# Optimization experiments

Hardware: AMD Instinct MI355X
Metric: run time of the kernel (lower is better)

## Reference

```python
import jax, jax.numpy as jnp
import numpy as np

B, T, NF, D = 512, 24, 81, 64
NH, HD = 4, 16
EPS = 1e-5


def _ln(x, g, b):
    m = x.mean(-1, keepdims=True)
    v = ((x - m) ** 2).mean(-1, keepdims=True)
    return (x - m) * jax.lax.rsqrt(v + EPS) * g + b


def _glu(h, w1, b1, w2, b2):
    return jax.nn.sigmoid(h @ w1 + b1) * (h @ w2 + b2)


def setup_inputs() -> dict:
    key = jax.random.key(0)
    ki = iter(jax.random.split(key, 64))

    def w(*shape):
        return jax.random.normal(next(ki), shape, jnp.float32) * 0.05

    FD = NF * D
    inp = {
        "x": jax.random.normal(next(ki), (B, T, NF), jnp.float32),
        # 81 per-feature GRNs, stacked along axis 0 (feature axis)
        "f_w1": w(NF, D), "f_b1": w(NF, D),
        "f_w2": w(NF, D, D), "f_b2": w(NF, D),
        "f_g1w": w(NF, D, D), "f_g1b": w(NF, D),
        "f_g2w": w(NF, D, D), "f_g2b": w(NF, D),
        "f_skw": w(NF, D), "f_skb": w(NF, D),
        "f_lng": jnp.ones((NF, D), jnp.float32), "f_lnb": jnp.zeros((NF, D), jnp.float32),
        # weight GRN: 5184 -> 64 -> 81
        "w_w1": w(FD, D), "w_b1": w(D),
        "w_w2": w(D, NF), "w_b2": w(NF),
        "w_g1w": w(NF, NF), "w_g1b": w(NF),
        "w_g2w": w(NF, NF), "w_g2b": w(NF),
        "w_skw": w(FD, NF), "w_skb": w(NF),
        "w_lng": jnp.ones((NF,), jnp.float32), "w_lnb": jnp.zeros((NF,), jnp.float32),
        # LSTM (torch layout: [4H, in], gate order i,f,g,o)
        "lstm_wih": w(4 * D, D), "lstm_whh": w(4 * D, D),
        "lstm_bih": w(4 * D), "lstm_bhh": w(4 * D),
        # post-lstm GLU + LN
        "pl_g1w": w(D, D), "pl_g1b": w(D), "pl_g2w": w(D, D), "pl_g2b": w(D),
        "pl_lng": jnp.ones((D,), jnp.float32), "pl_lnb": jnp.zeros((D,), jnp.float32),
        # MHA (in-proj packed q,k,v; weights stored [in, out])
        "attn_in_w": w(D, 3 * D), "attn_in_b": w(3 * D),
        "attn_out_w": w(D, D), "attn_out_b": w(D),
        # post-attn GLU + LN
        "pa_g1w": w(D, D), "pa_g1b": w(D), "pa_g2w": w(D, D), "pa_g2b": w(D),
        "pa_lng": jnp.ones((D,), jnp.float32), "pa_lnb": jnp.zeros((D,), jnp.float32),
        # feed-forward GRN (skip = identity since d_in == d_out)
        "ff_w1": w(D, 2 * D), "ff_b1": w(2 * D),
        "ff_w2": w(2 * D, D), "ff_b2": w(D),
        "ff_g1w": w(D, D), "ff_g1b": w(D), "ff_g2w": w(D, D), "ff_g2b": w(D),
        "ff_lng": jnp.ones((D,), jnp.float32), "ff_lnb": jnp.zeros((D,), jnp.float32),
        # output head
        "fc1_w": w(D, D), "fc1_b": w(D),
        "fc2_w": w(D, 6), "fc2_b": w(6),
    }
    return inp


def _forward(x, f_w1, f_b1, f_w2, f_b2, f_g1w, f_g1b, f_g2w, f_g2b, f_skw, f_skb,
             f_lng, f_lnb,
             w_w1, w_b1, w_w2, w_b2, w_g1w, w_g1b, w_g2w, w_g2b, w_skw, w_skb,
             w_lng, w_lnb,
             lstm_wih, lstm_whh, lstm_bih, lstm_bhh,
             pl_g1w, pl_g1b, pl_g2w, pl_g2b, pl_lng, pl_lnb,
             attn_in_w, attn_in_b, attn_out_w, attn_out_b,
             pa_g1w, pa_g1b, pa_g2w, pa_g2b, pa_lng, pa_lnb,
             ff_w1, ff_b1, ff_w2, ff_b2, ff_g1w, ff_g1b, ff_g2w, ff_g2b,
             ff_lng, ff_lnb,
             fc1_w, fc1_b, fc2_w, fc2_b):
    Bv, Tv = x.shape[0], x.shape[1]
    # --- VSN: 81 per-feature GRNs, vectorized over the feature axis ---
    h = jax.nn.elu(x[..., None] * f_w1 + f_b1)                    # [B,T,F,D]
    h = jnp.einsum('btfi,fio->btfo', h, f_w2) + f_b2
    h = jax.nn.sigmoid(jnp.einsum('btfi,fio->btfo', h, f_g1w) + f_g1b) \
        * (jnp.einsum('btfi,fio->btfo', h, f_g2w) + f_g2b)
    res = x[..., None] * f_skw + f_skb                            # skip: Linear(1,D)
    stacked = _ln(h + res, f_lng, f_lnb)                          # [B,T,F,D]
    flat = stacked.reshape(Bv, Tv, NF * D)
    # weight GRN -> softmax over features
    wh = jax.nn.elu(flat @ w_w1 + w_b1)
    wh = wh @ w_w2 + w_b2
    wh = _glu(wh, w_g1w, w_g1b, w_g2w, w_g2b)
    wnorm = _ln(wh + flat @ w_skw + w_skb, w_lng, w_lnb)
    weights = jax.nn.softmax(wnorm, axis=-1)                      # [B,T,F]
    selected = jnp.einsum('btfd,btf->btd', stacked, weights)      # [B,T,D]

    # --- LSTM encoder (single layer) ---
    def step(carry, xt):
        hp, cp = carry
        gates = xt @ lstm_wih.T + hp @ lstm_whh.T + lstm_bih + lstm_bhh
        i, f, g, o = jnp.split(gates, 4, axis=-1)
        c = jax.nn.sigmoid(f) * cp + jax.nn.sigmoid(i) * jnp.tanh(g)
        hn = jax.nn.sigmoid(o) * jnp.tanh(c)
        return (hn, c), hn

    h0 = jnp.zeros((Bv, D), x.dtype)
    _, hs = jax.lax.scan(step, (h0, h0), selected.transpose(1, 0, 2))
    lstm_out = hs.transpose(1, 0, 2)                              # [B,T,D]

    temporal = _ln(_glu(lstm_out, pl_g1w, pl_g1b, pl_g2w, pl_g2b) + selected,
                   pl_lng, pl_lnb)

    # --- Multi-head self-attention ---
    qkv = temporal @ attn_in_w + attn_in_b                        # [B,T,3D]
    q, k, v = jnp.split(qkv, 3, axis=-1)

    def heads(t):
        return t.reshape(Bv, Tv, NH, HD).transpose(0, 2, 1, 3)

    q, k, v = heads(q), heads(k), heads(v)
    scores = jnp.einsum('bhqd,bhkd->bhqk', q, k) / jnp.sqrt(jnp.float32(HD))
    a = jax.nn.softmax(scores, axis=-1)
    ao = jnp.einsum('bhqk,bhkd->bhqd', a, v).transpose(0, 2, 1, 3).reshape(Bv, Tv, D)
    attn_out = ao @ attn_out_w + attn_out_b

    enriched = _ln(_glu(attn_out, pa_g1w, pa_g1b, pa_g2w, pa_g2b) + temporal,
                   pa_lng, pa_lnb)

    # --- FF GRN (identity skip) ---
    fh = jax.nn.elu(enriched @ ff_w1 + ff_b1)
    fh = fh @ ff_w2 + ff_b2
    fh = _glu(fh, ff_g1w, ff_g1b, ff_g2w, ff_g2b)
    out = _ln(fh + enriched, ff_lng, ff_lnb)

    pooled = out.mean(axis=1)                                     # [B,D]
    return jax.nn.relu(pooled @ fc1_w + fc1_b) @ fc2_w + fc2_b    # [B,6]


def reference(x, f_w1, f_b1, f_w2, f_b2, f_g1w, f_g1b, f_g2w, f_g2b, f_skw, f_skb,
              f_lng, f_lnb,
              w_w1, w_b1, w_w2, w_b2, w_g1w, w_g1b, w_g2w, w_g2b, w_skw, w_skb,
              w_lng, w_lnb,
              lstm_wih, lstm_whh, lstm_bih, lstm_bhh,
              pl_g1w, pl_g1b, pl_g2w, pl_g2b, pl_lng, pl_lnb,
              attn_in_w, attn_in_b, attn_out_w, attn_out_b,
              pa_g1w, pa_g1b, pa_g2w, pa_g2b, pa_lng, pa_lnb,
              ff_w1, ff_b1, ff_w2, ff_b2, ff_g1w, ff_g1b, ff_g2w, ff_g2b,
              ff_lng, ff_lnb,
              fc1_w, fc1_b, fc2_w, fc2_b):
    return _forward(x, f_w1, f_b1, f_w2, f_b2, f_g1w, f_g1b, f_g2w, f_g2b, f_skw,
                    f_skb, f_lng, f_lnb, w_w1, w_b1, w_w2, w_b2, w_g1w, w_g1b,
                    w_g2w, w_g2b, w_skw, w_skb, w_lng, w_lnb, lstm_wih, lstm_whh,
                    lstm_bih, lstm_bhh, pl_g1w, pl_g1b, pl_g2w, pl_g2b, pl_lng,
                    pl_lnb, attn_in_w, attn_in_b, attn_out_w, attn_out_b, pa_g1w,
                    pa_g1b, pa_g2w, pa_g2b, pa_lng, pa_lnb, ff_w1, ff_b1, ff_w2,
                    ff_b2, ff_g1w, ff_g1b, ff_g2w, ff_g2b, ff_lng, ff_lnb, fc1_w,
                    fc1_b, fc2_w, fc2_b)
```

## Files before the change

kernel.cpp:

```cpp
#include <hip/hip_runtime.h>
#include <hip/hip_bf16.h>
#include <math.h>

constexpr int BB   = 512;
constexpr int TSEQ = 24;
constexpr int NF   = 81;
constexpr int DD   = 64;
constexpr int MTOT = BB * TSEQ;
constexpr int FDIM = NF * DD;
constexpr int KS   = 6;
constexpr int KSL  = 864;
constexpr int NW   = 160;
constexpr int NT   = 6;
constexpr float LN_EPS = 1e-5f;

typedef __attribute__((ext_vector_type(8))) short short8v;
typedef __attribute__((ext_vector_type(4))) float f32x4;

static __device__ __forceinline__ float sigmoidf_(float x) {
    return __builtin_amdgcn_rcpf(1.f + __expf(-x));
}
static __device__ __forceinline__ float eluf_(float x) {
    return x > 0.f ? x : (__expf(x) - 1.f);
}
// ... 403 lines not shown
            for (int rg = 0; rg < 4; ++rg)
                acc[rg][cf] = __builtin_amdgcn_mfma_f32_16x16x32_bf16(af[rg], bf, acc[rg][cf], 0, 0, 0);
        }
    }
    #pragma unroll
    for (int rg = 0; rg < 4; ++rg)
        #pragma unroll
        for (int cf = 0; cf < 4; ++cf)
            #pragma unroll
            for (int j = 0; j < 4; ++j) {
                int r = rg*16 + lg*4 + j, c = w*64 + cf*16 + lr;
                xW[(size_t)(m0 + r) * 256 + c] = acc[rg][cf][j] + vbs[c];
            }
}

__global__ void lstm_prep_kernel(
    const float* __restrict__ whh, float* __restrict__ whhT)
{
    int id = blockIdx.x * 256 + threadIdx.x;
    if (id < 16384) {
        int i = id >> 8, j = id & 255;
        whhT[id] = whh[j*64 + i];
    }
}

__global__ __launch_bounds__(256) void lstm_kernel(
    const float* __restrict__ xW, const float* __restrict__ whhT,
    float* __restrict__ out)
{
    __shared__ float sh[64];
    __shared__ float sg[256];
    const int t = threadIdx.x;
    const int b = blockIdx.x;

    float wreg[64];
    #pragma unroll
    for (int i = 0; i < 64; ++i) wreg[i] = whhT[i*256 + t];

    if (t < 64) sh[t] = 0.f;
    float c_reg = 0.f;

    float xnext = xW[((size_t)b * TSEQ + 0) * 256 + t];
    __syncthreads();

    for (int tt = 0; tt < TSEQ; ++tt) {
        float acc = xnext;
        if (tt + 1 < TSEQ)
            xnext = xW[((size_t)b * TSEQ + tt + 1) * 256 + t];
        #pragma unroll
        for (int i = 0; i < 64; ++i) acc += sh[i] * wreg[i];
        sg[t] = acc;
        __syncthreads();
        if (t < 64) {
            float gi = sg[t], gf = sg[64 + t], gg = sg[128 + t], go = sg[192 + t];
            c_reg = sigmoidf_(gf) * c_reg + sigmoidf_(gi) * ftanh_(gg);
            float hn = sigmoidf_(go) * ftanh_(c_reg);
            sh[t] = hn;
            out[((size_t)b * TSEQ + tt) * 64 + t] = hn;
        }
        __syncthreads();
    }
}

__global__ __launch_bounds__(256) void fused_pl_qkv_kernel(
    const float* __restrict__ in, const float* __restrict__ res,
    const float* __restrict__ g1w, const float* __restrict__ g1b,
    const float* __restrict__ g2w, const float* __restrict__ g2b,
    const float* __restrict__ lng, const float* __restrict__ lnb,
    const float* __restrict__ wqkv, const float* __restrict__ bqkv,
    float* __restrict__ outf, float* __restrict__ qkv)
{
    const int m0 = blockIdx.x * 32;
    const int t = threadIdx.x;
    const int w = t >> 6, l = t & 63, lr = l & 15, lg = l >> 4;
    __shared__ __align__(16) unsigned short hA[32 * 72];
    __shared__ __align__(16) unsigned char U[27648];
    unsigned short* Wt0 = (unsigned short*)U;
    unsigned short* Wt1 = (unsigned short*)(U + 9216);
    float* yA = (float*)U;
    unsigned short* Wq = (unsigned short*)U;
    __shared__ float vg1b[64], vg2b[64], vlng[64], vlnb[64], vbq[192];

    if (t < 64) { vg1b[t] = g1b[t]; vg2b[t] = g2b[t]; vlng[t] = lng[t]; vlnb[t] = lnb[t]; }
    if (t < 192) vbq[t] = bqkv[t];
    #pragma unroll
    for (int p = 0; p < 8; ++p) {
        int e = t + 256 * p; int r = e >> 6, d = e & 63;
        hA[r*72 + d] = f2bf(in[(size_t)(m0 + r) * 64 + d]);
    }
    #pragma unroll
    for (int p = 0; p < 16; ++p) {
        int e = t + 256 * p; int k = e >> 6, c = e & 63;
        Wt0[c*72 + k] = f2bf(g1w[k*64 + c]);
        Wt1[c*72 + k] = f2bf(g2w[k*64 + c]);
    }
    __syncthreads();

    f32x4 aA[2], aB[2];
    #pragma unroll
    for (int rg = 0; rg < 2; ++rg) { aA[rg] = (f32x4){0.f,0.f,0.f,0.f}; aB[rg] = (f32x4){0.f,0.f,0.f,0.f}; }
    #pragma unroll
    for (int ks = 0; ks < 2; ++ks) {
        short8v b0f = *(const short8v*)&Wt0[(w*16 + lr)*72 + ks*32 + lg*8];
        short8v b1f = *(const short8v*)&Wt1[(w*16 + lr)*72 + ks*32 + lg*8];
        #pragma unroll
        for (int rg = 0; rg < 2; ++rg) {
            short8v af = *(const short8v*)&hA[(rg*16 + lr)*72 + ks*32 + lg*8];
            aA[rg] = __builtin_amdgcn_mfma_f32_16x16x32_bf16(af, b0f, aA[rg], 0, 0, 0);
            aB[rg] = __builtin_amdgcn_mfma_f32_16x16x32_bf16(af, b1f, aB[rg], 0, 0, 0);
        }
    }
    float yv[2][4];
    #pragma unroll
    for (int rg = 0; rg < 2; ++rg)
        #pragma unroll
        for (int j = 0; j < 4; ++j) {
            int r = rg*16 + lg*4 + j, c = w*16 + lr;
            float sg = sigmoidf_(aA[rg][j] + vg1b[c]);
            yv[rg][j] = sg * (aB[rg][j] + vg2b[c]) + res[(size_t)(m0 + r) * 64 + c];
        }
    __syncthreads();

    #pragma unroll
    for (int rg = 0; rg < 2; ++rg)
        #pragma unroll
        for (int j = 0; j < 4; ++j) {
            int r = rg*16 + lg*4 + j, c = w*16 + lr;
            yA[r*68 + c] = yv[rg][j];
        }
    __syncthreads();

    const int tr = t >> 4, tc = t & 15;
    #pragma unroll
    for (int a = 0; a < 2; ++a) {
        const int r = tr + 16*a;
        float4 v4 = *(const float4*)&yA[r*68 + tc*4];
        float part = v4.x + v4.y + v4.z + v4.w;
        #pragma unroll
        for (int off = 1; off < 16; off <<= 1) part += __shfl_xor(part, off);
        const float mean = part * (1.f / 64.f);
        float d0 = v4.x - mean, d1 = v4.y - mean, d2 = v4.z - mean, d3 = v4.w - mean;
        float vp = d0*d0 + d1*d1 + d2*d2 + d3*d3;
        #pragma unroll
        for (int off = 1; off < 16; off <<= 1) vp += __shfl_xor(vp, off);
        const float inv = rsqrtf(vp * (1.f / 64.f) + LN_EPS);
        const int c0 = tc * 4;
        float4 ov;
        ov.x = d0 * inv * vlng[c0+0] + vlnb[c0+0];
        ov.y = d1 * inv * vlng[c0+1] + vlnb[c0+1];
        ov.z = d2 * inv * vlng[c0+2] + vlnb[c0+2];
        ov.w = d3 * inv * vlng[c0+3] + vlnb[c0+3];
        *(float4*)&outf[(size_t)(m0 + r) * 64 + c0] = ov;
        ushort4 ob;
        ob.x = f2bf(ov.x); ob.y = f2bf(ov.y); ob.z = f2bf(ov.z); ob.w = f2bf(ov.w);
        *(ushort4*)&hA[r*72 + c0] = ob;
    }
    __syncthreads();

    #pragma unroll
    for (int p = 0; p < 48; ++p) {
        int e = t + 256 * p; int c = e >> 6, k = e & 63;
        Wq[c*72 + k] = f2bf(wqkv[(size_t)k * 192 + c]);
    }
    __syncthreads();

    f32x4 acc[2][3];
    #pragma unroll
    for (int rg = 0; rg < 2; ++rg)
        #pragma unroll
        for (int cf = 0; cf < 3; ++cf) acc[rg][cf] = (f32x4){0.f,0.f,0.f,0.f};
    #pragma unroll
    for (int ks = 0; ks < 2; ++ks) {
        short8v af[2];
        #pragma unroll
        for (int rg = 0; rg < 2; ++rg)
            af[rg] = *(const short8v*)&hA[(rg*16 + lr)*72 + ks*32 + lg*8];
        #pragma unroll
        for (int cf = 0; cf < 3; ++cf) {
            short8v bf = *(const short8v*)&Wq[(w*48 + cf*16 + lr)*72 + ks*32 + lg*8];
            #pragma unroll
            for (int rg = 0; rg < 2; ++rg)
                acc[rg][cf] = __builtin_amdgcn_mfma_f32_16x16x32_bf16(af[rg], bf, acc[rg][cf], 0, 0, 0);
        }
    }
    #pragma unroll
    for (int rg = 0; rg < 2; ++rg)
        #pragma unroll
        for (int cf = 0; cf < 3; ++cf)
            #pragma unroll
            for (int j = 0; j < 4; ++j) {
                int r = rg*16 + lg*4 + j, c = w*48 + cf*16 + lr;
                qkv[(size_t)(m0 + r) * 192 + c] = acc[rg][cf][j] + vbq[c];
            }
}

__global__ __launch_bounds__(256) void attn_kernel(
    const float* __restrict__ qkv, __hip_bfloat16* __restrict__ ao)
{
    const int b = blockIdx.x;
    const int h = threadIdx.x >> 6, l = threadIdx.x & 63;
    __shared__ float sq[4][24][16], sk[4][24][16], sv[4][24][16], sp[4][24][24];
    #pragma unroll
    for (int p = 0; p < 6; ++p) {
        int e = l + 64 * p; int ti = e >> 4, d = e & 15;
        size_t base = ((size_t)(b * TSEQ + ti)) * 192 + h * 16 + d;
        sq[h][ti][d] = qkv[base];
        sk[h][ti][d] = qkv[base + 64];
        sv[h][ti][d] = qkv[base + 128];
    }
    __syncthreads();
    #pragma unroll
    for (int p = 0; p < 9; ++p) {
        int e = l + 64 * p; int i = e / 24, j = e - i * 24;
        float s = 0.f;
        #pragma unroll
        for (int d = 0; d < 16; ++d) s += sq[h][i][d] * sk[h][j][d];
        sp[h][i][j] = s * 0.25f;
    }
    __syncthreads();
    if (l < 24) {
        float mx = -1e30f;
        for (int j = 0; j < 24; ++j) mx = fmaxf(mx, sp[h][l][j]);
        float s = 0.f;
        for (int j = 0; j < 24; ++j) { float e = __expf(sp[h][l][j] - mx); sp[h][l][j] = e; s += e; }
        float inv = __builtin_amdgcn_rcpf(s);
        for (int j = 0; j < 24; ++j) sp[h][l][j] *= inv;
    }
    __syncthreads();
    #pragma unroll
    for (int p = 0; p < 6; ++p) {
        int e = l + 64 * p; int ti = e >> 4, d = e & 15;
        float s = 0.f;
        #pragma unroll
        for (int j = 0; j < 24; ++j) s += sp[h][ti][j] * sv[h][j][d];
        ao[((size_t)(b * TSEQ + ti)) * 64 + h * 16 + d] = __float2bfloat16(s);
    }
}

__global__ __launch_bounds__(256) void fused_paff_kernel(
    const __hip_bfloat16* __restrict__ ao, const float* __restrict__ res_t,
    const float* __restrict__ wout, const float* __restrict__ bout,
    const float* __restrict__ pg1w, const float* __restrict__ pg1b,
    const float* __restrict__ pg2w, const float* __restrict__ pg2b,
    const float* __restrict__ plng, const float* __restrict__ plnb,
    const float* __restrict__ fw1, const float* __restrict__ fb1,
    const float* __restrict__ fw2, const float* __restrict__ fb2,
    const float* __restrict__ fg1w, const float* __restrict__ fg1b,
    const float* __restrict__ fg2w, const float* __restrict__ fg2b,
    const float* __restrict__ flng, const float* __restrict__ flnb,
    float* __restrict__ escratch, float* __restrict__ outln)
{
    const int m0 = blockIdx.x * 32;
    const int t = threadIdx.x;
    const int w = t >> 6, l = t & 63, lr = l & 15, lg = l >> 4;
    __shared__ __align__(16) unsigned short hA[32 * 72];
    __shared__ __align__(16) unsigned short hB[32 * 136];
    __shared__ __align__(16) unsigned char U1[18432];
    __shared__ __align__(16) unsigned char U2[17408];
    unsigned short* Wt0 = (unsigned short*)U1;
    unsigned short* Wt1 = (unsigned short*)(U1 + 9216);
    unsigned short* W1t = (unsigned short*)U1;
    unsigned short* W2t = (unsigned short*)U2;
    float* yA = (float*)U2;
    __shared__ float vob[64], vp1b[64], vp2b[64], vplg[64], vplb[64];
    __shared__ float vf1b[128], vf2b[64], vfg1b[64], vfg2b[64], vflg[64], vflb[64];

    if (t < 64) {
        vob[t] = bout[t]; vp1b[t] = pg1b[t]; vp2b[t] = pg2b[t];
        vplg[t] = plng[t]; vplb[t] = plnb[t];
        vf2b[t] = fb2[t]; vfg1b[t] = fg1b[t]; vfg2b[t] = fg2b[t];
        vflg[t] = flng[t]; vflb[t] = flnb[t];
    }
    if (t < 128) vf1b[t] = fb1[t];
    #pragma unroll
    for (int p = 0; p < 8; ++p) {
        int e = t + 256 * p; int r = e >> 6, d = e & 63;
        hA[r*72 + d] = *(const unsigned short*)&ao[(size_t)(m0 + r) * 64 + d];
    }
    #pragma unroll
    for (int p = 0; p < 16; ++p) {
        int e = t + 256 * p; int k = e >> 6, c = e & 63;
        Wt0[c*72 + k] = f2bf(wout[k*64 + c]);
    }
    __syncthreads();

    f32x4 acc1[2];
    #pragma unroll
    for (int rg = 0; rg < 2; ++rg) acc1[rg] = (f32x4){0.f,0.f,0.f,0.f};
    #pragma unroll
    for (int ks = 0; ks < 2; ++ks) {
        short8v bf = *(const short8v*)&Wt0[(w*16 + lr)*72 + ks*32 + lg*8];
        #pragma unroll
        for (int rg = 0; rg < 2; ++rg) {
            short8v af = *(const short8v*)&hA[(rg*16 + lr)*72 + ks*32 + lg*8];
            acc1[rg] = __builtin_amdgcn_mfma_f32_16x16x32_bf16(af, bf, acc1[rg], 0, 0, 0);
        }
    }
    #pragma unroll
    for (int p = 0; p < 16; ++p) {
        int e = t + 256 * p; int k = e >> 6, c = e & 63;
        Wt1[c*72 + k] = f2bf(pg1w[k*64 + c]);
    }
    __syncthreads();

    #pragma unroll
    for (int rg = 0; rg < 2; ++rg)
        #pragma unroll
        for (int j = 0; j < 4; ++j) {
            int r = rg*16 + lg*4 + j, c = w*16 + lr;
            hA[r*72 + c] = f2bf(acc1[rg][j] + vob[c]);
        }
    #pragma unroll
    for (int p = 0; p < 16; ++p) {
        int e = t + 256 * p; int k = e >> 6, c = e & 63;
        Wt0[c*72 + k] = f2bf(pg2w[k*64 + c]);
    }
    __syncthreads();

    f32x4 aA[2], aB[2];
    #pragma unroll
    for (int rg = 0; rg < 2; ++rg) { aA[rg] = (f32x4){0.f,0.f,0.f,0.f}; aB[rg] = (f32x4){0.f,0.f,0.f,0.f}; }
    #pragma unroll
    for (int ks = 0; ks < 2; ++ks) {
        short8v b1f = *(const short8v*)&Wt1[(w*16 + lr)*72 + ks*32 + lg*8];
        short8v b2f = *(const short8v*)&Wt0[(w*16 + lr)*72 + ks*32 + lg*8];
        #pragma unroll
        for (int rg = 0; rg < 2; ++rg) {
            short8v af = *(const short8v*)&hA[(rg*16 + lr)*72 + ks*32 + lg*8];
            aA[rg] = __builtin_amdgcn_mfma_f32_16x16x32_bf16(af, b1f, aA[rg], 0, 0, 0);
            aB[rg] = __builtin_amdgcn_mfma_f32_16x16x32_bf16(af, b2f, aB[rg], 0, 0, 0);
        }
    }
    float yv[2][4];
    #pragma unroll
    for (int rg = 0; rg < 2; ++rg)
        #pragma unroll
        for (int j = 0; j < 4; ++j) {
            int r = rg*16 + lg*4 + j, c = w*16 + lr;
            float sg = sigmoidf_(aA[rg][j] + vp1b[c]);
            yv[rg][j] = sg * (aB[rg][j] + vp2b[c]) + res_t[(size_t)(m0 + r) * 64 + c];
        }
    __syncthreads();

    #pragma unroll
    for (int rg = 0; rg < 2; ++rg)
        #pragma unroll
        for (int j = 0; j < 4; ++j) {
            int r = rg*16 + lg*4 + j, c = w*16 + lr;
            yA[r*68 + c] = yv[rg][j];
        }
    __syncthreads();

    const int tr = t >> 4, tc = t & 15;
    #pragma unroll
    for (int a = 0; a < 2; ++a) {
        const int r = tr + 16*a;
        float4 v4 = *(const float4*)&yA[r*68 + tc*4];
        float part = v4.x + v4.y + v4.z + v4.w;
        #pragma unroll
        for (int off = 1; off < 16; off <<= 1) part += __shfl_xor(part, off);
        const float mean = part * (1.f / 64.f);
        float d0 = v4.x - mean, d1 = v4.y - mean, d2 = v4.z - mean, d3 = v4.w - mean;
        float vp = d0*d0 + d1*d1 + d2*d2 + d3*d3;
        #pragma unroll
        for (int off = 1; off < 16; off <<= 1) vp += __shfl_xor(vp, off);
        const float inv = rsqrtf(vp * (1.f / 64.f) + LN_EPS);
        const int c0 = tc * 4;
        float4 ov;
        ov.x = d0 * inv * vplg[c0+0] + vplb[c0+0];
        ov.y = d1 * inv * vplg[c0+1] + vplb[c0+1];
        ov.z = d2 * inv * vplg[c0+2] + vplb[c0+2];
        ov.w = d3 * inv * vplg[c0+3] + vplb[c0+3];
        *(float4*)&escratch[(size_t)(m0 + r) * 64 + c0] = ov;
        ushort4 ob;
        ob.x = f2bf(ov.x); ob.y = f2bf(ov.y); ob.z = f2bf(ov.z); ob.w = f2bf(ov.w);
        *(ushort4*)&hA[r*72 + c0] = ob;
    }
    __syncthreads();

    #pragma unroll
    for (int p = 0; p < 32; ++p) {
        int e = t + 256 * p; int k = e >> 7, c = e & 127;
        W1t[c*72 + k] = f2bf(fw1[(size_t)k * 128 + c]);
    }
    __syncthreads();

    f32x4 accf[2][2];
    #pragma unroll
// ... 65 lines not shown
    for (int ks = 0; ks < 2; ++ks) {
        short8v b1f = *(const short8v*)&Wt0[(w*16 + lr)*72 + ks*32 + lg*8];
        short8v b2f = *(const short8v*)&Wt1[(w*16 + lr)*72 + ks*32 + lg*8];
        #pragma unroll
        for (int rg = 0; rg < 2; ++rg) {
            short8v af = *(const short8v*)&hA[(rg*16 + lr)*72 + ks*32 + lg*8];
            aA[rg] = __builtin_amdgcn_mfma_f32_16x16x32_bf16(af, b1f, aA[rg], 0, 0, 0);
            aB[rg] = __builtin_amdgcn_mfma_f32_16x16x32_bf16(af, b2f, aB[rg], 0, 0, 0);
        }
    }
    #pragma unroll
    for (int rg = 0; rg < 2; ++rg)
        #pragma unroll
        for (int j = 0; j < 4; ++j) {
            int r = rg*16 + lg*4 + j, c = w*16 + lr;
            float sg = sigmoidf_(aA[rg][j] + vfg1b[c]);
            yv[rg][j] = sg * (aB[rg][j] + vfg2b[c]) + escratch[(size_t)(m0 + r) * 64 + c];
        }
    __syncthreads();

    #pragma unroll
    for (int rg = 0; rg < 2; ++rg)
        #pragma unroll
        for (int j = 0; j < 4; ++j) {
            int r = rg*16 + lg*4 + j, c = w*16 + lr;
            yA[r*68 + c] = yv[rg][j];
        }
    __syncthreads();

    #pragma unroll
    for (int a = 0; a < 2; ++a) {
        const int r = tr + 16*a;
// ... 1 lines not shown
        float part = v4.x + v4.y + v4.z + v4.w;
        #pragma unroll
        for (int off = 1; off < 16; off <<= 1) part += __shfl_xor(part, off);
        const float mean = part * (1.f / 64.f);
        float d0 = v4.x - mean, d1 = v4.y - mean, d2 = v4.z - mean, d3 = v4.w - mean;
        float vp = d0*d0 + d1*d1 + d2*d2 + d3*d3;
        #pragma unroll
        for (int off = 1; off < 16; off <<= 1) vp += __shfl_xor(vp, off);
        const float inv = rsqrtf(vp * (1.f / 64.f) + LN_EPS);
        const int c0 = tc * 4;
        float4 ov;
        ov.x = d0 * inv * vflg[c0+0] + vflb[c0+0];
        ov.y = d1 * inv * vflg[c0+1] + vflb[c0+1];
        ov.z = d2 * inv * vflg[c0+2] + vflb[c0+2];
        ov.w = d3 * inv * vflg[c0+3] + vflb[c0+3];
        *(float4*)&outln[(size_t)(m0 + r) * 64 + c0] = ov;
    }
}

__global__ __launch_bounds__(64) void head_kernel(
    const float* __restrict__ outln,
    const float* __restrict__ fc1_w, const float* __restrict__ fc1_b,
    const float* __restrict__ fc2_w, const float* __restrict__ fc2_b,
    float* __restrict__ out)
{
    const int b = blockIdx.x, l = threadIdx.x;
    __shared__ float sp[64];
    float s = 0.f;
    #pragma unroll
    for (int tt = 0; tt < TSEQ; ++tt) s += outln[((size_t)(b * TSEQ + tt)) * 64 + l];
    sp[l] = s * (1.f / 24.f);
    __syncthreads();
    float a = fc1_b[l];
    for (int k = 0; k < 64; ++k) a += sp[k] * fc1_w[k*64 + l];
    float f1 = fmaxf(a, 0.f);
    #pragma unroll
    for (int j = 0; j < 6; ++j) {
        float p = f1 * fc2_w[l*6 + j];
        #pragma unroll
        for (int off = 32; off; off >>= 1) p += __shfl_xor(p, off);
        if (l == 0) out[b*6 + j] = p + fc2_b[j];
    }
}

extern "C" void kernel_launch(void* const* d_in, const int* in_sizes, int n_in,
                              void* d_out, int out_size, void* d_ws, size_t ws_size,
                              hipStream_t stream)
{
    const float* x        = (const float*)d_in[0];
    const float* f_w1     = (const float*)d_in[1];
    const float* f_b1     = (const float*)d_in[2];
    const float* f_w2     = (const float*)d_in[3];
    const float* f_b2     = (const float*)d_in[4];
    const float* f_g1w    = (const float*)d_in[5];
    const float* f_g1b    = (const float*)d_in[6];
    const float* f_g2w    = (const float*)d_in[7];
// ... 41 lines not shown
    const float* ff_g1w   = (const float*)d_in[49];
    const float* ff_g1b   = (const float*)d_in[50];
    const float* ff_g2w   = (const float*)d_in[51];
    const float* ff_g2b   = (const float*)d_in[52];
    const float* ff_lng   = (const float*)d_in[53];
    const float* ff_lnb   = (const float*)d_in[54];
    const float* fc1_w    = (const float*)d_in[55];
    const float* fc1_b    = (const float*)d_in[56];
    const float* fc2_w    = (const float*)d_in[57];
    const float* fc2_b    = (const float*)d_in[58];

    float* ws = (float*)d_ws;

    size_t o = 0;
    const size_t o_S0   = o; o += (size_t)MTOT * 256;
    const size_t o_A    = o; o += (size_t)MTOT * 64;
    const size_t o_Bf   = o; o += (size_t)MTOT * 64;
    const size_t o_Cf   = o; o += (size_t)MTOT * 64;
    const size_t o_Df   = o; o += (size_t)MTOT * 64;
    const size_t o_F    = o; o += (size_t)MTOT * 128;
    const size_t o_whhT = o; o += 16384;
    const size_t unionP2 = o;

    const size_t o_ab = o_F;

    const size_t persist = (size_t)MTOT * 177;
    int mc = 0;
    {
        const int cands[4] = {12288, 6144, 3072, 1536};
        for (int ci = 0; ci < 4; ++ci) {
            const size_t c = (size_t)cands[ci];
            size_t overlay = c * FDIM / 2 + (size_t)KS * c * NW + c * 81
                           + (size_t)NW * FDIM / 2;
            size_t A = overlay > unionP2 ? overlay : unionP2;
            if ((A + persist) * sizeof(float) <= ws_size) { mc = cands[ci]; break; }
        }
        if (mc == 0) return;
    }
    const size_t ovl_partial = (size_t)mc * FDIM / 2;
// ... 13 lines not shown

    for (int mb = 0; mb < MTOT; mb += mc) {
        __hip_bfloat16* chunk = (__hip_bfloat16*)ws;
        vsn_kernel<<<dim3((mc / 64) / NT, NF), blk, 0, stream>>>(
            ws + o_xt + mb, f_w1, f_b1, f_w2, f_b2, f_g1w, f_g1b,
            f_g2w, f_g2b, f_skw, f_skb, f_lng, f_lnb, chunk);
        wgemm_kernel<<<dim3(mc / 32, KS), dim3(64), 0, stream>>>(
            chunk, (const unsigned short*)(ws + ovl_wcat), ws + ovl_partial, mc);
        wtail_kernel<<<dim3(mc / 16), blk, 0, stream>>>(
            ws + ovl_partial, chunk, w_b1, w_skb, w_w2, w_b2, w_g1w, w_g1b,
            w_g2w, w_g2b, w_lng, w_lnb,
            ws + o_sel + (size_t)mb * 64,
            (__hip_bfloat16*)(ws + o_selb) + (size_t)mb * 64, mc);
    }

    lstm_prep_kernel<<<dim3(64), blk, 0, stream>>>(lstm_whh, ws + o_whhT);
    xw_kernel<<<dim3(MTOT / 64), blk, 0, stream>>>(
        (const __hip_bfloat16*)(ws + o_selb), lstm_wih, lstm_bih, lstm_bhh, ws + o_S0);
    lstm_kernel<<<dim3(BB), blk, 0, stream>>>(ws + o_S0, ws + o_whhT, ws + o_A);
    fused_pl_qkv_kernel<<<dim3(MTOT / 32), blk, 0, stream>>>(
        ws + o_A, ws + o_sel, pl_g1w, pl_g1b, pl_g2w, pl_g2b, pl_lng, pl_lnb,
        attn_in_w, attn_in_b, ws + o_Df, ws + o_S0);
    attn_kernel<<<dim3(BB), blk, 0, stream>>>(
        ws + o_S0, (__hip_bfloat16*)(ws + o_ab));
    fused_paff_kernel<<<dim3(MTOT / 32), blk, 0, stream>>>(
        (const __hip_bfloat16*)(ws + o_ab), ws + o_Df,
        attn_out_w, attn_out_b, pa_g1w, pa_g1b, pa_g2w, pa_g2b, pa_lng, pa_lnb,
        ff_w1, ff_b1, ff_w2, ff_b2, ff_g1w, ff_g1b, ff_g2w, ff_g2b,
        ff_lng, ff_lnb, ws + o_Bf, ws + o_Cf);
    head_kernel<<<dim3(BB), dim3(64), 0, stream>>>(
        ws + o_Cf, fc1_w, fc1_b, fc2_w, fc2_b, (float*)d_out);
}
```

Before: 355.6 us.

## Fuse LSTM, post-LSTM GLU, attention, feed-forward and head into one per-batch kernel

Replaces five kernels (LSTM, post-LSTM GLU+QKV, attention, post-attention/FF GRN, head) with one kernel that runs one block per batch element and keeps every intermediate in shared memory. The hidden state goes straight into a bf16 tile padded to 32 rows, and residuals stay in LDS, so the global round trips and launches between stages disappear. It also drops the separate W_hh transpose kernel by loading W_hh rows directly into registers. In exchange only 512 blocks do the dense GEMM stages (previously 384 blocks of 32 rows each), and the larger LDS footprint plus 64 weight registers per thread may reduce occupancy. Every block also reconverts all the weight matrices.

```diff
diff --git a/kernel.cpp b/kernel.cpp
--- a/kernel.cpp
+++ b/kernel.cpp
@@ -441,39 +441,76 @@
             }
 }
 
-__global__ void lstm_prep_kernel(
-    const float* __restrict__ whh, float* __restrict__ whhT)
-{
-    int id = blockIdx.x * 256 + threadIdx.x;
-    if (id < 16384) {
-        int i = id >> 8, j = id & 255;
-        whhT[id] = whh[j*64 + i];
-    }
-}
-
-__global__ __launch_bounds__(256) void lstm_kernel(
-    const float* __restrict__ xW, const float* __restrict__ whhT,
+__global__ __launch_bounds__(256) void batch_kernel(
+    const float* __restrict__ xW, const float* __restrict__ whh,
+    const float* __restrict__ sel,
+    const float* __restrict__ pg1w, const float* __restrict__ pg1b,
+    const float* __restrict__ pg2w, const float* __restrict__ pg2b,
+    const float* __restrict__ plng, const float* __restrict__ plnb,
+    const float* __restrict__ wqkv, const float* __restrict__ bqkv,
+    const float* __restrict__ wout, const float* __restrict__ bout,
+    const float* __restrict__ ag1w, const float* __restrict__ ag1b,
+    const float* __restrict__ ag2w, const float* __restrict__ ag2b,
+    const float* __restrict__ alng, const float* __restrict__ alnb,
+    const float* __restrict__ fw1, const float* __restrict__ fb1,
+    const float* __restrict__ fw2, const float* __restrict__ fb2,
+    const float* __restrict__ fg1w, const float* __restrict__ fg1b,
+    const float* __restrict__ fg2w, const float* __restrict__ fg2b,
+    const float* __restrict__ flng, const float* __restrict__ flnb,
+    const float* __restrict__ fc1_w, const float* __restrict__ fc1_b,
+    const float* __restrict__ fc2_w, const float* __restrict__ fc2_b,
     float* __restrict__ out)
 {
-    __shared__ float sh[64];
-    __shared__ float sg[256];
-    const int t = threadIdx.x;
-    const int b = blockIdx.x;
+    const int b  = blockIdx.x;
+    const int m0 = b * TSEQ;
+    const int t  = threadIdx.x;
+    const int w  = t >> 6, l = t & 63, lr = l & 15, lg = l >> 4;
+    const int tr = t >> 4, tc = t & 15;
+
+    __shared__ float tmp[32 * 68];
+    __shared__ float enr[32 * 68];
+    __shared__ __align__(16) unsigned short hA[32 * 72];
+    __shared__ __align__(16) unsigned short hB[32 * 136];
+    __shared__ __align__(16) unsigned char U[35840];
+    __shared__ float sh[64], sg[256];
+    __shared__ float vpg1b[64], vpg2b[64], vplg[64], vplb[64], vbq[192];
+    __shared__ float vob[64], vag1b[64], vag2b[64], valg[64], valb[64];
+    __shared__ float vf1b[128], vf2b[64], vfg1b[64], vfg2b[64], vflg[64], vflb[64];
+
+    unsigned short* Wt0 = (unsigned short*)U;
+    unsigned short* Wt1 = (unsigned short*)(U + 9216);
+    float*          yA  = (float*)(U + 18432);
+    unsigned short* Wq  = (unsigned short*)U;
+    float* sq = (float*)U;
+    float* sk = (float*)(U + 6144);
+    float* sv = (float*)(U + 12288);
+    float* sp = (float*)(U + 18432);
+    unsigned short* W1t = (unsigned short*)U;
+    unsigned short* W2t = (unsigned short*)(U + 18432);
+
+    if (t < 64) {
+        vpg1b[t] = pg1b[t]; vpg2b[t] = pg2b[t]; vplg[t] = plng[t]; vplb[t] = plnb[t];
+        vob[t] = bout[t]; vag1b[t] = ag1b[t]; vag2b[t] = ag2b[t];
+        valg[t] = alng[t]; valb[t] = alnb[t];
+        vf2b[t] = fb2[t]; vfg1b[t] = fg1b[t]; vfg2b[t] = fg2b[t];
+        vflg[t] = flng[t]; vflb[t] = flnb[t];
+    }
+    if (t < 192) vbq[t] = bqkv[t];
+    if (t < 128) vf1b[t] = fb1[t];
+    for (int e = t; e < 8 * 72; e += 256) hA[24*72 + e] = 0;
 
     float wreg[64];
     #pragma unroll
-    for (int i = 0; i < 64; ++i) wreg[i] = whhT[i*256 + t];
-
+    for (int i = 0; i < 64; ++i) wreg[i] = whh[t*64 + i];
     if (t < 64) sh[t] = 0.f;
     float c_reg = 0.f;
-
-    float xnext = xW[((size_t)b * TSEQ + 0) * 256 + t];
+    float xnext = xW[(size_t)m0 * 256 + t];
     __syncthreads();
 
     for (int tt = 0; tt < TSEQ; ++tt) {
         float acc = xnext;
         if (tt + 1 < TSEQ)
-            xnext = xW[((size_t)b * TSEQ + tt + 1) * 256 + t];
+            xnext = xW[(size_t)(m0 + tt + 1) * 256 + t];
         #pragma unroll
         for (int i = 0; i < 64; ++i) acc += sh[i] * wreg[i];
         sg[t] = acc;
@@ -483,43 +520,16 @@
             c_reg = sigmoidf_(gf) * c_reg + sigmoidf_(gi) * ftanh_(gg);
             float hn = sigmoidf_(go) * ftanh_(c_reg);
             sh[t] = hn;
-            out[((size_t)b * TSEQ + tt) * 64 + t] = hn;
+            hA[tt*72 + t] = f2bf(hn);
         }
         __syncthreads();
     }
-}
-
-__global__ __launch_bounds__(256) void fused_pl_qkv_kernel(
-    const float* __restrict__ in, const float* __restrict__ res,
-    const float* __restrict__ g1w, const float* __restrict__ g1b,
-    const float* __restrict__ g2w, const float* __restrict__ g2b,
-    const float* __restrict__ lng, const float* __restrict__ lnb,
-    const float* __restrict__ wqkv, const float* __restrict__ bqkv,
-    float* __restrict__ outf, float* __restrict__ qkv)
-{
-    const int m0 = blockIdx.x * 32;
-    const int t = threadIdx.x;
-    const int w = t >> 6, l = t & 63, lr = l & 15, lg = l >> 4;
-    __shared__ __align__(16) unsigned short hA[32 * 72];
-    __shared__ __align__(16) unsigned char U[27648];
-    unsigned short* Wt0 = (unsigned short*)U;
-    unsigned short* Wt1 = (unsigned short*)(U + 9216);
-    float* yA = (float*)U;
-    unsigned short* Wq = (unsigned short*)U;
-    __shared__ float vg1b[64], vg2b[64], vlng[64], vlnb[64], vbq[192];
-
-    if (t < 64) { vg1b[t] = g1b[t]; vg2b[t] = g2b[t]; vlng[t] = lng[t]; vlnb[t] = lnb[t]; }
-    if (t < 192) vbq[t] = bqkv[t];
-    #pragma unroll
-    for (int p = 0; p < 8; ++p) {
-        int e = t + 256 * p; int r = e >> 6, d = e & 63;
-        hA[r*72 + d] = f2bf(in[(size_t)(m0 + r) * 64 + d]);
-    }
+
     #pragma unroll
     for (int p = 0; p < 16; ++p) {
         int e = t + 256 * p; int k = e >> 6, c = e & 63;
-        Wt0[c*72 + k] = f2bf(g1w[k*64 + c]);
-        Wt1[c*72 + k] = f2bf(g2w[k*64 + c]);
+        Wt0[c*72 + k] = f2bf(pg1w[k*64 + c]);
+        Wt1[c*72 + k] = f2bf(pg2w[k*64 + c]);
     }
     __syncthreads();
 
@@ -543,8 +553,9 @@
         #pragma unroll
         for (int j = 0; j < 4; ++j) {
             int r = rg*16 + lg*4 + j, c = w*16 + lr;
-            float sg = sigmoidf_(aA[rg][j] + vg1b[c]);
-            yv[rg][j] = sg * (aB[rg][j] + vg2b[c]) + res[(size_t)(m0 + r) * 64 + c];
+            size_t rrow = (size_t)(m0 + r); if (rrow >= MTOT) rrow = MTOT - 1;
+            float sgv = sigmoidf_(aA[rg][j] + vpg1b[c]);
+            yv[rg][j] = sgv * (aB[rg][j] + vpg2b[c]) + sel[rrow * 64 + c];
         }
     __syncthreads();
 
@@ -557,228 +568,6 @@
         }
     __syncthreads();
 
-    const int tr = t >> 4, tc = t & 15;
-    #pragma unroll
-    for (int a = 0; a < 2; ++a) {
-        const int r = tr + 16*a;
-        float4 v4 = *(const float4*)&yA[r*68 + tc*4];
-        float part = v4.x + v4.y + v4.z + v4.w;
-        #pragma unroll
-        for (int off = 1; off < 16; off <<= 1) part += __shfl_xor(part, off);
-        const float mean = part * (1.f / 64.f);
-        float d0 = v4.x - mean, d1 = v4.y - mean, d2 = v4.z - mean, d3 = v4.w - mean;
-        float vp = d0*d0 + d1*d1 + d2*d2 + d3*d3;
-        #pragma unroll
-        for (int off = 1; off < 16; off <<= 1) vp += __shfl_xor(vp, off);
-        const float inv = rsqrtf(vp * (1.f / 64.f) + LN_EPS);
-        const int c0 = tc * 4;
-        float4 ov;
-        ov.x = d0 * inv * vlng[c0+0] + vlnb[c0+0];
-        ov.y = d1 * inv * vlng[c0+1] + vlnb[c0+1];
-        ov.z = d2 * inv * vlng[c0+2] + vlnb[c0+2];
-        ov.w = d3 * inv * vlng[c0+3] + vlnb[c0+3];
-        *(float4*)&outf[(size_t)(m0 + r) * 64 + c0] = ov;
-        ushort4 ob;
-        ob.x = f2bf(ov.x); ob.y = f2bf(ov.y); ob.z = f2bf(ov.z); ob.w = f2bf(ov.w);
-        *(ushort4*)&hA[r*72 + c0] = ob;
-    }
-    __syncthreads();
-
-    #pragma unroll
-    for (int p = 0; p < 48; ++p) {
-        int e = t + 256 * p; int c = e >> 6, k = e & 63;
-        Wq[c*72 + k] = f2bf(wqkv[(size_t)k * 192 + c]);
-    }
-    __syncthreads();
-
-    f32x4 acc[2][3];
-    #pragma unroll
-    for (int rg = 0; rg < 2; ++rg)
-        #pragma unroll
-        for (int cf = 0; cf < 3; ++cf) acc[rg][cf] = (f32x4){0.f,0.f,0.f,0.f};
-    #pragma unroll
-    for (int ks = 0; ks < 2; ++ks) {
-        short8v af[2];
-        #pragma unroll
-        for (int rg = 0; rg < 2; ++rg)
-            af[rg] = *(const short8v*)&hA[(rg*16 + lr)*72 + ks*32 + lg*8];
-        #pragma unroll
-        for (int cf = 0; cf < 3; ++cf) {
-            short8v bf = *(const short8v*)&Wq[(w*48 + cf*16 + lr)*72 + ks*32 + lg*8];
-            #pragma unroll
-            for (int rg = 0; rg < 2; ++rg)
-                acc[rg][cf] = __builtin_amdgcn_mfma_f32_16x16x32_bf16(af[rg], bf, acc[rg][cf], 0, 0, 0);
-        }
-    }
-    #pragma unroll
-    for (int rg = 0; rg < 2; ++rg)
-        #pragma unroll
-        for (int cf = 0; cf < 3; ++cf)
-            #pragma unroll
-            for (int j = 0; j < 4; ++j) {
-                int r = rg*16 + lg*4 + j, c = w*48 + cf*16 + lr;
-                qkv[(size_t)(m0 + r) * 192 + c] = acc[rg][cf][j] + vbq[c];
-            }
-}
-
-__global__ __launch_bounds__(256) void attn_kernel(
-    const float* __restrict__ qkv, __hip_bfloat16* __restrict__ ao)
-{
-    const int b = blockIdx.x;
-    const int h = threadIdx.x >> 6, l = threadIdx.x & 63;
-    __shared__ float sq[4][24][16], sk[4][24][16], sv[4][24][16], sp[4][24][24];
-    #pragma unroll
-    for (int p = 0; p < 6; ++p) {
-        int e = l + 64 * p; int ti = e >> 4, d = e & 15;
-        size_t base = ((size_t)(b * TSEQ + ti)) * 192 + h * 16 + d;
-        sq[h][ti][d] = qkv[base];
-        sk[h][ti][d] = qkv[base + 64];
-        sv[h][ti][d] = qkv[base + 128];
-    }
-    __syncthreads();
-    #pragma unroll
-    for (int p = 0; p < 9; ++p) {
-        int e = l + 64 * p; int i = e / 24, j = e - i * 24;
-        float s = 0.f;
-        #pragma unroll
-        for (int d = 0; d < 16; ++d) s += sq[h][i][d] * sk[h][j][d];
-        sp[h][i][j] = s * 0.25f;
-    }
-    __syncthreads();
-    if (l < 24) {
-        float mx = -1e30f;
-        for (int j = 0; j < 24; ++j) mx = fmaxf(mx, sp[h][l][j]);
-        float s = 0.f;
-        for (int j = 0; j < 24; ++j) { float e = __expf(sp[h][l][j] - mx); sp[h][l][j] = e; s += e; }
-        float inv = __builtin_amdgcn_rcpf(s);
-        for (int j = 0; j < 24; ++j) sp[h][l][j] *= inv;
-    }
-    __syncthreads();
-    #pragma unroll
-    for (int p = 0; p < 6; ++p) {
-        int e = l + 64 * p; int ti = e >> 4, d = e & 15;
-        float s = 0.f;
-        #pragma unroll
-        for (int j = 0; j < 24; ++j) s += sp[h][ti][j] * sv[h][j][d];
-        ao[((size_t)(b * TSEQ + ti)) * 64 + h * 16 + d] = __float2bfloat16(s);
-    }
-}
-
-__global__ __launch_bounds__(256) void fused_paff_kernel(
-    const __hip_bfloat16* __restrict__ ao, const float* __restrict__ res_t,
-    const float* __restrict__ wout, const float* __restrict__ bout,
-    const float* __restrict__ pg1w, const float* __restrict__ pg1b,
-    const float* __restrict__ pg2w, const float* __restrict__ pg2b,
-    const float* __restrict__ plng, const float* __restrict__ plnb,
-    const float* __restrict__ fw1, const float* __restrict__ fb1,
-    const float* __restrict__ fw2, const float* __restrict__ fb2,
-    const float* __restrict__ fg1w, const float* __restrict__ fg1b,
-    const float* __restrict__ fg2w, const float* __restrict__ fg2b,
-    const float* __restrict__ flng, const float* __restrict__ flnb,
-    float* __restrict__ escratch, float* __restrict__ outln)
-{
-    const int m0 = blockIdx.x * 32;
-    const int t = threadIdx.x;
-    const int w = t >> 6, l = t & 63, lr = l & 15, lg = l >> 4;
-    __shared__ __align__(16) unsigned short hA[32 * 72];
-    __shared__ __align__(16) unsigned short hB[32 * 136];
-    __shared__ __align__(16) unsigned char U1[18432];
-    __shared__ __align__(16) unsigned char U2[17408];
-    unsigned short* Wt0 = (unsigned short*)U1;
-    unsigned short* Wt1 = (unsigned short*)(U1 + 9216);
-    unsigned short* W1t = (unsigned short*)U1;
-    unsigned short* W2t = (unsigned short*)U2;
-    float* yA = (float*)U2;
-    __shared__ float vob[64], vp1b[64], vp2b[64], vplg[64], vplb[64];
-    __shared__ float vf1b[128], vf2b[64], vfg1b[64], vfg2b[64], vflg[64], vflb[64];
-
-    if (t < 64) {
-        vob[t] = bout[t]; vp1b[t] = pg1b[t]; vp2b[t] = pg2b[t];
-        vplg[t] = plng[t]; vplb[t] = plnb[t];
-        vf2b[t] = fb2[t]; vfg1b[t] = fg1b[t]; vfg2b[t] = fg2b[t];
-        vflg[t] = flng[t]; vflb[t] = flnb[t];
-    }
-    if (t < 128) vf1b[t] = fb1[t];
-    #pragma unroll
-    for (int p = 0; p < 8; ++p) {
-        int e = t + 256 * p; int r = e >> 6, d = e & 63;
-        hA[r*72 + d] = *(const unsigned short*)&ao[(size_t)(m0 + r) * 64 + d];
-    }
-    #pragma unroll
-    for (int p = 0; p < 16; ++p) {
-        int e = t + 256 * p; int k = e >> 6, c = e & 63;
-        Wt0[c*72 + k] = f2bf(wout[k*64 + c]);
-    }
-    __syncthreads();
-
-    f32x4 acc1[2];
-    #pragma unroll
-    for (int rg = 0; rg < 2; ++rg) acc1[rg] = (f32x4){0.f,0.f,0.f,0.f};
-    #pragma unroll
-    for (int ks = 0; ks < 2; ++ks) {
-        short8v bf = *(const short8v*)&Wt0[(w*16 + lr)*72 + ks*32 + lg*8];
-        #pragma unroll
-        for (int rg = 0; rg < 2; ++rg) {
-            short8v af = *(const short8v*)&hA[(rg*16 + lr)*72 + ks*32 + lg*8];
-            acc1[rg] = __builtin_amdgcn_mfma_f32_16x16x32_bf16(af, bf, acc1[rg], 0, 0, 0);
-        }
-    }
-    #pragma unroll
-    for (int p = 0; p < 16; ++p) {
-        int e = t + 256 * p; int k = e >> 6, c = e & 63;
-        Wt1[c*72 + k] = f2bf(pg1w[k*64 + c]);
-    }
-    __syncthreads();
-
-    #pragma unroll
-    for (int rg = 0; rg < 2; ++rg)
-        #pragma unroll
-        for (int j = 0; j < 4; ++j) {
-            int r = rg*16 + lg*4 + j, c = w*16 + lr;
-            hA[r*72 + c] = f2bf(acc1[rg][j] + vob[c]);
-        }
-    #pragma unroll
-    for (int p = 0; p < 16; ++p) {
-        int e = t + 256 * p; int k = e >> 6, c = e & 63;
-        Wt0[c*72 + k] = f2bf(pg2w[k*64 + c]);
-    }
-    __syncthreads();
-
-    f32x4 aA[2], aB[2];
-    #pragma unroll
-    for (int rg = 0; rg < 2; ++rg) { aA[rg] = (f32x4){0.f,0.f,0.f,0.f}; aB[rg] = (f32x4){0.f,0.f,0.f,0.f}; }
-    #pragma unroll
-    for (int ks = 0; ks < 2; ++ks) {
-        short8v b1f = *(const short8v*)&Wt1[(w*16 + lr)*72 + ks*32 + lg*8];
-        short8v b2f = *(const short8v*)&Wt0[(w*16 + lr)*72 + ks*32 + lg*8];
-        #pragma unroll
-        for (int rg = 0; rg < 2; ++rg) {
-            short8v af = *(const short8v*)&hA[(rg*16 + lr)*72 + ks*32 + lg*8];
-            aA[rg] = __builtin_amdgcn_mfma_f32_16x16x32_bf16(af, b1f, aA[rg], 0, 0, 0);
-            aB[rg] = __builtin_amdgcn_mfma_f32_16x16x32_bf16(af, b2f, aB[rg], 0, 0, 0);
-        }
-    }
-    float yv[2][4];
-    #pragma unroll
-    for (int rg = 0; rg < 2; ++rg)
-        #pragma unroll
-        for (int j = 0; j < 4; ++j) {
-            int r = rg*16 + lg*4 + j, c = w*16 + lr;
-            float sg = sigmoidf_(aA[rg][j] + vp1b[c]);
-            yv[rg][j] = sg * (aB[rg][j] + vp2b[c]) + res_t[(size_t)(m0 + r) * 64 + c];
-        }
-    __syncthreads();
-
-    #pragma unroll
-    for (int rg = 0; rg < 2; ++rg)
-        #pragma unroll
-        for (int j = 0; j < 4; ++j) {
-            int r = rg*16 + lg*4 + j, c = w*16 + lr;
-            yA[r*68 + c] = yv[rg][j];
-        }
-    __syncthreads();
-
-    const int tr = t >> 4, tc = t & 15;
     #pragma unroll
     for (int a = 0; a < 2; ++a) {
         const int r = tr + 16*a;
@@ -798,7 +587,177 @@
         ov.y = d1 * inv * vplg[c0+1] + vplb[c0+1];
         ov.z = d2 * inv * vplg[c0+2] + vplb[c0+2];
         ov.w = d3 * inv * vplg[c0+3] + vplb[c0+3];
-        *(float4*)&escratch[(size_t)(m0 + r) * 64 + c0] = ov;
+        *(float4*)&tmp[r*68 + c0] = ov;
+        ushort4 ob;
+        ob.x = f2bf(ov.x); ob.y = f2bf(ov.y); ob.z = f2bf(ov.z); ob.w = f2bf(ov.w);
+        *(ushort4*)&hA[r*72 + c0] = ob;
+    }
+    __syncthreads();
+
+    #pragma unroll
+    for (int p = 0; p < 48; ++p) {
+        int e = t + 256 * p; int c = e >> 6, k = e & 63;
+        Wq[c*72 + k] = f2bf(wqkv[(size_t)k * 192 + c]);
+    }
+    __syncthreads();
+
+    f32x4 accq[2][3];
+    #pragma unroll
+    for (int rg = 0; rg < 2; ++rg)
+        #pragma unroll
+        for (int cf = 0; cf < 3; ++cf) accq[rg][cf] = (f32x4){0.f,0.f,0.f,0.f};
+    #pragma unroll
+    for (int ks = 0; ks < 2; ++ks) {
+        short8v af[2];
+        #pragma unroll
+        for (int rg = 0; rg < 2; ++rg)
+            af[rg] = *(const short8v*)&hA[(rg*16 + lr)*72 + ks*32 + lg*8];
+        #pragma unroll
+        for (int cf = 0; cf < 3; ++cf) {
+            short8v bf = *(const short8v*)&Wq[(w*48 + cf*16 + lr)*72 + ks*32 + lg*8];
+            #pragma unroll
+            for (int rg = 0; rg < 2; ++rg)
+                accq[rg][cf] = __builtin_amdgcn_mfma_f32_16x16x32_bf16(af[rg], bf, accq[rg][cf], 0, 0, 0);
+        }
+    }
+    __syncthreads();
+
+    #pragma unroll
+    for (int rg = 0; rg < 2; ++rg)
+        #pragma unroll
+        for (int cf = 0; cf < 3; ++cf)
+            #pragma unroll
+            for (int j = 0; j < 4; ++j) {
+                int r = rg*16 + lg*4 + j, c = w*48 + cf*16 + lr;
+                if (r < TSEQ) {
+                    float val = accq[rg][cf][j] + vbq[c];
+                    int seg = c >> 6, hh = (c & 63) >> 4, dd = c & 15;
+                    float* dst = (seg == 0) ? sq : (seg == 1 ? sk : sv);
+                    dst[(hh*24 + r)*16 + dd] = val;
+                }
+            }
+    __syncthreads();
+
+    #pragma unroll
+    for (int p = 0; p < 9; ++p) {
+        int e = l + 64 * p; int i = e / 24, j2 = e - i * 24;
+        float s = 0.f;
+        #pragma unroll
+        for (int d = 0; d < 16; ++d) s += sq[(w*24 + i)*16 + d] * sk[(w*24 + j2)*16 + d];
+        sp[(w*24 + i)*24 + j2] = s * 0.25f;
+    }
+    __syncthreads();
+    if (l < 24) {
+        float mx = -1e30f;
+        for (int j = 0; j < 24; ++j) mx = fmaxf(mx, sp[(w*24 + l)*24 + j]);
+        float s = 0.f;
+        for (int j = 0; j < 24; ++j) { float e = __expf(sp[(w*24 + l)*24 + j] - mx); sp[(w*24 + l)*24 + j] = e; s += e; }
+        float inv = __builtin_amdgcn_rcpf(s);
+        for (int j = 0; j < 24; ++j) sp[(w*24 + l)*24 + j] *= inv;
+    }
+    __syncthreads();
+    #pragma unroll
+    for (int p = 0; p < 6; ++p) {
+        int e = l + 64 * p; int ti = e >> 4, d = e & 15;
+        float s = 0.f;
+        #pragma unroll
+        for (int j = 0; j < 24; ++j) s += sp[(w*24 + ti)*24 + j] * sv[(w*24 + j)*16 + d];
+        hA[ti*72 + w*16 + d] = f2bf(s);
+    }
+    __syncthreads();
+
+    #pragma unroll
+    for (int p = 0; p < 16; ++p) {
+        int e = t + 256 * p; int k = e >> 6, c = e & 63;
+        Wt0[c*72 + k] = f2bf(wout[k*64 + c]);
+    }
+    __syncthreads();
+
+    f32x4 acc1[2];
+    #pragma unroll
+    for (int rg = 0; rg < 2; ++rg) acc1[rg] = (f32x4){0.f,0.f,0.f,0.f};
+    #pragma unroll
+    for (int ks = 0; ks < 2; ++ks) {
+        short8v bf = *(const short8v*)&Wt0[(w*16 + lr)*72 + ks*32 + lg*8];
+        #pragma unroll
+        for (int rg = 0; rg < 2; ++rg) {
+            short8v af = *(const short8v*)&hA[(rg*16 + lr)*72 + ks*32 + lg*8];
+            acc1[rg] = __builtin_amdgcn_mfma_f32_16x16x32_bf16(af, bf, acc1[rg], 0, 0, 0);
+        }
+    }
+    #pragma unroll
+    for (int p = 0; p < 16; ++p) {
+        int e = t + 256 * p; int k = e >> 6, c = e & 63;
+        Wt1[c*72 + k] = f2bf(ag1w[k*64 + c]);
+    }
+    __syncthreads();
+
+    #pragma unroll
+    for (int rg = 0; rg < 2; ++rg)
+        #pragma unroll
+        for (int j = 0; j < 4; ++j) {
+            int r = rg*16 + lg*4 + j, c = w*16 + lr;
+            hA[r*72 + c] = f2bf(acc1[rg][j] + vob[c]);
+        }
+    #pragma unroll
+    for (int p = 0; p < 16; ++p) {
+        int e = t + 256 * p; int k = e >> 6, c = e & 63;
+        Wt0[c*72 + k] = f2bf(ag2w[k*64 + c]);
+    }
+    __syncthreads();
+
+    #pragma unroll
+    for (int rg = 0; rg < 2; ++rg) { aA[rg] = (f32x4){0.f,0.f,0.f,0.f}; aB[rg] = (f32x4){0.f,0.f,0.f,0.f}; }
+    #pragma unroll
+    for (int ks = 0; ks < 2; ++ks) {
+        short8v b1f = *(const short8v*)&Wt1[(w*16 + lr)*72 + ks*32 + lg*8];
+        short8v b2f = *(const short8v*)&Wt0[(w*16 + lr)*72 + ks*32 + lg*8];
+        #pragma unroll
+        for (int rg = 0; rg < 2; ++rg) {
+            short8v af = *(const short8v*)&hA[(rg*16 + lr)*72 + ks*32 + lg*8];
+            aA[rg] = __builtin_amdgcn_mfma_f32_16x16x32_bf16(af, b1f, aA[rg], 0, 0, 0);
+            aB[rg] = __builtin_amdgcn_mfma_f32_16x16x32_bf16(af, b2f, aB[rg], 0, 0, 0);
+        }
+    }
+    #pragma unroll
+    for (int rg = 0; rg < 2; ++rg)
+        #pragma unroll
+        for (int j = 0; j < 4; ++j) {
+            int r = rg*16 + lg*4 + j, c = w*16 + lr;
+            float sgv = sigmoidf_(aA[rg][j] + vag1b[c]);
+            yv[rg][j] = sgv * (aB[rg][j] + vag2b[c]) + tmp[r*68 + c];
+        }
+    __syncthreads();
+
+    #pragma unroll
+    for (int rg = 0; rg < 2; ++rg)
+        #pragma unroll
+        for (int j = 0; j < 4; ++j) {
+            int r = rg*16 + lg*4 + j, c = w*16 + lr;
+            yA[r*68 + c] = yv[rg][j];
+        }
+    __syncthreads();
+
+    #pragma unroll
+    for (int a = 0; a < 2; ++a) {
+        const int r = tr + 16*a;
+        float4 v4 = *(const float4*)&yA[r*68 + tc*4];
+        float part = v4.x + v4.y + v4.z + v4.w;
+        #pragma unroll
+        for (int off = 1; off < 16; off <<= 1) part += __shfl_xor(part, off);
+        const float mean = part * (1.f / 64.f);
+        float d0 = v4.x - mean, d1 = v4.y - mean, d2 = v4.z - mean, d3 = v4.w - mean;
+        float vp = d0*d0 + d1*d1 + d2*d2 + d3*d3;
+        #pragma unroll
+        for (int off = 1; off < 16; off <<= 1) vp += __shfl_xor(vp, off);
+        const float inv = rsqrtf(vp * (1.f / 64.f) + LN_EPS);
+        const int c0 = tc * 4;
+        float4 ov;
+        ov.x = d0 * inv * valg[c0+0] + valb[c0+0];
+        ov.y = d1 * inv * valg[c0+1] + valb[c0+1];
+        ov.z = d2 * inv * valg[c0+2] + valb[c0+2];
+        ov.w = d3 * inv * valg[c0+3] + valb[c0+3];
+        *(float4*)&enr[r*68 + c0] = ov;
         ushort4 ob;
         ob.x = f2bf(ov.x); ob.y = f2bf(ov.y); ob.z = f2bf(ov.z); ob.w = f2bf(ov.w);
         *(ushort4*)&hA[r*72 + c0] = ob;
@@ -894,8 +853,8 @@
         #pragma unroll
         for (int j = 0; j < 4; ++j) {
             int r = rg*16 + lg*4 + j, c = w*16 + lr;
-            float sg = sigmoidf_(aA[rg][j] + vfg1b[c]);
-            yv[rg][j] = sg * (aB[rg][j] + vfg2b[c]) + escratch[(size_t)(m0 + r) * 64 + c];
+            float sgv = sigmoidf_(aA[rg][j] + vfg1b[c]);
+            yv[rg][j] = sgv * (aB[rg][j] + vfg2b[c]) + enr[r*68 + c];
         }
     __syncthreads();
 
@@ -927,32 +886,28 @@
         ov.y = d1 * inv * vflg[c0+1] + vflb[c0+1];
         ov.z = d2 * inv * vflg[c0+2] + vflb[c0+2];
         ov.w = d3 * inv * vflg[c0+3] + vflb[c0+3];
-        *(float4*)&outln[(size_t)(m0 + r) * 64 + c0] = ov;
-    }
-}
-
-__global__ __launch_bounds__(64) void head_kernel(
-    const float* __restrict__ outln,
-    const float* __restrict__ fc1_w, const float* __restrict__ fc1_b,
-    const float* __restrict__ fc2_w, const float* __restrict__ fc2_b,
-    float* __restrict__ out)
-{
-    const int b = blockIdx.x, l = threadIdx.x;
-    __shared__ float sp[64];
-    float s = 0.f;
-    #pragma unroll
-    for (int tt = 0; tt < TSEQ; ++tt) s += outln[((size_t)(b * TSEQ + tt)) * 64 + l];
-    sp[l] = s * (1.f / 24.f);
-    __syncthreads();
-    float a = fc1_b[l];
-    for (int k = 0; k < 64; ++k) a += sp[k] * fc1_w[k*64 + l];
-    float f1 = fmaxf(a, 0.f);
-    #pragma unroll
-    for (int j = 0; j < 6; ++j) {
-        float p = f1 * fc2_w[l*6 + j];
-        #pragma unroll
-        for (int off = 32; off; off >>= 1) p += __shfl_xor(p, off);
-        if (l == 0) out[b*6 + j] = p + fc2_b[j];
+        *(float4*)&tmp[r*68 + c0] = ov;
+    }
+    __syncthreads();
+
+    if (t < 64) {
+        float s = 0.f;
+        #pragma unroll
+        for (int tt = 0; tt < TSEQ; ++tt) s += tmp[tt*68 + t];
+        sh[t] = s * (1.f / 24.f);
+    }
+    __syncthreads();
+    if (t < 64) {
+        float a = fc1_b[t];
+        for (int k = 0; k < 64; ++k) a += sh[k] * fc1_w[k*64 + t];
+        float f1 = fmaxf(a, 0.f);
+        #pragma unroll
+        for (int j = 0; j < 6; ++j) {
+            float p = f1 * fc2_w[t*6 + j];
+            #pragma unroll
+            for (int off = 32; off; off >>= 1) p += __shfl_xor(p, off);
+            if (t == 0) out[b*6 + j] = p + fc2_b[j];
+        }
     }
 }
 
@@ -1024,15 +979,13 @@
 
     size_t o = 0;
     const size_t o_S0   = o; o += (size_t)MTOT * 256;
-    const size_t o_A    = o; o += (size_t)MTOT * 64;
-    const size_t o_Bf   = o; o += (size_t)MTOT * 64;
-    const size_t o_Cf   = o; o += (size_t)MTOT * 64;
-    const size_t o_Df   = o; o += (size_t)MTOT * 64;
-    const size_t o_F    = o; o += (size_t)MTOT * 128;
-    const size_t o_whhT = o; o += 16384;
+    o += (size_t)MTOT * 64;
+    o += (size_t)MTOT * 64;
+    o += (size_t)MTOT * 64;
+    o += (size_t)MTOT * 64;
+    o += (size_t)MTOT * 128;
+    o += 16384;
     const size_t unionP2 = o;
-
-    const size_t o_ab = o_F;
 
     const size_t persist = (size_t)MTOT * 177;
     int mc = 0;
@@ -1076,20 +1029,13 @@
             (__hip_bfloat16*)(ws + o_selb) + (size_t)mb * 64, mc);
     }
 
-    lstm_prep_kernel<<<dim3(64), blk, 0, stream>>>(lstm_whh, ws + o_whhT);
     xw_kernel<<<dim3(MTOT / 64), blk, 0, stream>>>(
         (const __hip_bfloat16*)(ws + o_selb), lstm_wih, lstm_bih, lstm_bhh, ws + o_S0);
-    lstm_kernel<<<dim3(BB), blk, 0, stream>>>(ws + o_S0, ws + o_whhT, ws + o_A);
-    fused_pl_qkv_kernel<<<dim3(MTOT / 32), blk, 0, stream>>>(
-        ws + o_A, ws + o_sel, pl_g1w, pl_g1b, pl_g2w, pl_g2b, pl_lng, pl_lnb,
-        attn_in_w, attn_in_b, ws + o_Df, ws + o_S0);
-    attn_kernel<<<dim3(BB), blk, 0, stream>>>(
-        ws + o_S0, (__hip_bfloat16*)(ws + o_ab));
-    fused_paff_kernel<<<dim3(MTOT / 32), blk, 0, stream>>>(
-        (const __hip_bfloat16*)(ws + o_ab), ws + o_Df,
-        attn_out_w, attn_out_b, pa_g1w, pa_g1b, pa_g2w, pa_g2b, pa_lng, pa_lnb,
+    batch_kernel<<<dim3(BB), blk, 0, stream>>>(
+        ws + o_S0, lstm_whh, ws + o_sel,
+        pl_g1w, pl_g1b, pl_g2w, pl_g2b, pl_lng, pl_lnb,
+        attn_in_w, attn_in_b, attn_out_w, attn_out_b,
+        pa_g1w, pa_g1b, pa_g2w, pa_g2b, pa_lng, pa_lnb,
         ff_w1, ff_b1, ff_w2, ff_b2, ff_g1w, ff_g1b, ff_g2w, ff_g2b,
-        ff_lng, ff_lnb, ws + o_Bf, ws + o_Cf);
-    head_kernel<<<dim3(BB), dim3(64), 0, stream>>>(
-        ws + o_Cf, fc1_w, fc1_b, fc2_w, fc2_b, (float*)d_out);
-}
+        ff_lng, ff_lnb, fc1_w, fc1_b, fc2_w, fc2_b, (float*)d_out);
+}
```

New measurement: 366.7 us. 1.03x slower.
